# Performance work log

Hardware: AMD Instinct MI355X
Metric: run time of the kernel (lower is better)

The kernel has to match this reference:

```python
import jax, jax.numpy as jnp
import numpy as np


def setup_inputs() -> dict:
    key = jax.random.key(0)
    k1, k2 = jax.random.split(key)
    x = jax.random.normal(k1, (16, 512, 64, 64), dtype=jnp.float32)
    gamma = jax.random.normal(k2, (1,), dtype=jnp.float32) * 0.05  # 'random_normal' init
    return {"x": x, "gamma": gamma}


def reference(x, gamma):
    # x: (B, C, H, W); code path is channels_last, C taken from x.shape[1]
    B, C, H, W = x.shape
    N = H * W
    # Reshape((-1, C)) is a flat row-major reshape -> (B, N, C)
    q = x.reshape(B, N, C)  # query == key == value (same tensor)
    # energy = matmul(query, key, transpose_a=True) -> (B, C, C)
    energy = jnp.einsum('bnc,bnd->bcd', q, q)
    # reduce_max(energy, axis=1, keepdims=True)[0]: max over axis 1 then take
    # FIRST BATCH element -> shape (1, C), broadcast against (B, C, C)
    mx = jnp.max(energy, axis=1, keepdims=True)[0]  # (1, C)
    energy_2 = mx - energy  # (B, C, C)
    # Keras Activation('softmax') -> softmax over last axis
    attention = jax.nn.softmax(energy_2, axis=-1)  # (B, C, C)
    # matmul(attention, value, transpose_b=True): (B,C,C) @ (B,C,N) -> (B,C,N)
    out = jnp.einsum('bcd,bnd->bcn', attention, q)
    # Reshape back to x.shape[1:] = (C, H, W) (flat reshape, N = H*W)
    out = out.reshape(B, C, H, W)
    return gamma * out + x
```

## Files before the change

kernel.cpp:

```cpp
#include <hip/hip_runtime.h>
#include <cstdint>

#define B_DIM 16
#define C_DIM 512
#define N_DIM 4096

typedef __bf16 bf16x8 __attribute__((ext_vector_type(8)));
typedef unsigned short u16x8 __attribute__((ext_vector_type(8)));
typedef unsigned short u16x4 __attribute__((ext_vector_type(4)));
typedef float f32x4 __attribute__((ext_vector_type(4)));

__device__ __forceinline__ unsigned short f2bf_tr(float f) {
    return (unsigned short)(__float_as_uint(f) >> 16);
}
__device__ __forceinline__ bf16x8 as_bf(u16x8 v) {
    return __builtin_bit_cast(bf16x8, v);
}

#define BT 128
#define BK 32
#define BKP 40

__global__ __launch_bounds__(256) void gram_kernel(const float* __restrict__ x,
                                                   float* __restrict__ part, int kshift) {
    const int sk = 1 << kshift;
    const int s = blockIdx.z & (sk - 1);
    const int b = blockIdx.z >> kshift;
    static const int TI[10] = {0, 0, 0, 0, 1, 1, 1, 2, 2, 3};
    static const int TJ[10] = {0, 1, 2, 3, 1, 2, 3, 2, 3, 3};
    const int c0 = TI[blockIdx.x] * BT;
    const int d0 = TJ[blockIdx.x] * BT;
    const bool diag = (c0 == d0);

    const float* __restrict__ Q = x + (size_t)b * (N_DIM * C_DIM);
    float* __restrict__ E = part + ((size_t)s * B_DIM + b) * (C_DIM * C_DIM);

    __shared__ unsigned short lAh[BT][BKP];
    __shared__ unsigned short lAl[BT][BKP];
    __shared__ unsigned short lBh[BT][BKP];
    __shared__ unsigned short lBl[BT][BKP];

    const int tid = threadIdx.x;
    const int lane = tid & 63;
    const int w = tid >> 6;
    const int moff = (w & 1) * 64;
    const int noff = (w >> 1) * 64;
    const int frow = lane & 15;
    const int fk = (lane >> 4) * 8;

    f32x4 acc[4][4];
#pragma unroll
    for (int m = 0; m < 4; ++m)
#pragma unroll
        for (int n = 0; n < 4; ++n) acc[m][n] = (f32x4){0.f, 0.f, 0.f, 0.f};

    const int cc = tid & 127;
    const int kh = tid >> 7;

    const int klen = N_DIM >> kshift;
    const int kbeg = s * klen;
    const float* gA = Q + (size_t)(kbeg + kh * 16) * C_DIM + (c0 + cc);
    const float* gB = Q + (size_t)(kbeg + kh * 16) * C_DIM + (d0 + cc);

    const unsigned short(*pBh)[BKP] = diag ? lAh : lBh;
    const unsigned short(*pBl)[BKP] = diag ? lAl : lBl;

    for (int k0 = 0; k0 < klen; k0 += BK) {
        u16x8 vah[2], val[2], vbh[2], vbl[2];
#pragma unroll
        for (int i = 0; i < 16; ++i) {
            float fa = gA[(size_t)i * C_DIM];
            unsigned int ua = __float_as_uint(fa);
            unsigned short ah = (unsigned short)(ua >> 16);
            float rsa = fa - __uint_as_float(ua & 0xffff0000u);
            unsigned short al = (unsigned short)(__float_as_uint(rsa) >> 16);
            vah[i >> 3][i & 7] = ah;
            val[i >> 3][i & 7] = al;
        }
        if (!diag) {
#pragma unroll
            for (int i = 0; i < 16; ++i) {
                float fb = gB[(size_t)i * C_DIM];
                unsigned int ub = __float_as_uint(fb);
                unsigned short bh = (unsigned short)(ub >> 16);
                float rsb = fb - __uint_as_float(ub & 0xffff0000u);
                unsigned short bl = (unsigned short)(__float_as_uint(rsb) >> 16);
                vbh[i >> 3][i & 7] = bh;
                vbl[i >> 3][i & 7] = bl;
            }
        }
        gA += (size_t)BK * C_DIM;
        gB += (size_t)BK * C_DIM;

        __syncthreads();
        *(u16x8*)&lAh[cc][kh * 16]     = vah[0];
        *(u16x8*)&lAh[cc][kh * 16 + 8] = vah[1];
        *(u16x8*)&lAl[cc][kh * 16]     = val[0];
        *(u16x8*)&lAl[cc][kh * 16 + 8] = val[1];
        if (!diag) {
            *(u16x8*)&lBh[cc][kh * 16]     = vbh[0];
            *(u16x8*)&lBh[cc][kh * 16 + 8] = vbh[1];
            *(u16x8*)&lBl[cc][kh * 16]     = vbl[0];
            *(u16x8*)&lBl[cc][kh * 16 + 8] = vbl[1];
        }
        __syncthreads();

        bf16x8 fa_h[4], fa_l[4], fb_h[4], fb_l[4];
#pragma unroll
        for (int m = 0; m < 4; ++m) {
            fa_h[m] = as_bf(*(const u16x8*)&lAh[moff + m * 16 + frow][fk]);
            fa_l[m] = as_bf(*(const u16x8*)&lAl[moff + m * 16 + frow][fk]);
        }
#pragma unroll
        for (int n = 0; n < 4; ++n) {
            fb_h[n] = as_bf(*(const u16x8*)&pBh[noff + n * 16 + frow][fk]);
            fb_l[n] = as_bf(*(const u16x8*)&pBl[noff + n * 16 + frow][fk]);
        }
#pragma unroll
        for (int m = 0; m < 4; ++m)
#pragma unroll
            for (int n = 0; n < 4; ++n) {
                acc[m][n] = __builtin_amdgcn_mfma_f32_16x16x32_bf16(fa_h[m], fb_h[n], acc[m][n], 0, 0, 0);
                acc[m][n] = __builtin_amdgcn_mfma_f32_16x16x32_bf16(fa_h[m], fb_l[n], acc[m][n], 0, 0, 0);
                acc[m][n] = __builtin_amdgcn_mfma_f32_16x16x32_bf16(fa_l[m], fb_h[n], acc[m][n], 0, 0, 0);
            }
    }

#pragma unroll
    for (int m = 0; m < 4; ++m)
#pragma unroll
        for (int n = 0; n < 4; ++n) {
            const int r = c0 + moff + m * 16 + (lane >> 4) * 4;
            const int col = d0 + noff + n * 16 + frow;
#pragma unroll
            for (int i = 0; i < 4; ++i)
                E[(size_t)(r + i) * C_DIM + col] = acc[m][n][i];
        }
    if (!diag) {
#pragma unroll
        for (int m = 0; m < 4; ++m)
#pragma unroll
            for (int n = 0; n < 4; ++n) {
                const int r = c0 + moff + m * 16 + (lane >> 4) * 4;
                const int col = d0 + noff + n * 16 + frow;
#pragma unroll
                for (int i = 0; i < 4; ++i)
                    E[(size_t)col * C_DIM + (r + i)] = acc[m][n][i];
            }
    }
}

__global__ __launch_bounds__(256) void colmax1(const float* __restrict__ part,
                                               float* __restrict__ pmax, int sk) {
    const int d = blockIdx.x * 256 + threadIdx.x;
    const int cg = blockIdx.y;
    const size_t PS = (size_t)B_DIM * C_DIM * C_DIM;
    float m = -3.4e38f;
    for (int c = cg * 64; c < cg * 64 + 64; ++c) {
        float e = 0.f;
        for (int s = 0; s < sk; ++s) e += part[(size_t)s * PS + (size_t)c * C_DIM + d];
        m = fmaxf(m, e);
    }
    pmax[cg * C_DIM + d] = m;
}

__global__ __launch_bounds__(256) void colmax2(const float* __restrict__ pmax,
                                               float* __restrict__ mx) {
    const int d = blockIdx.x * 256 + threadIdx.x;
    float m = pmax[d];
#pragma unroll
    for (int g = 1; g < 8; ++g) m = fmaxf(m, pmax[g * C_DIM + d]);
    mx[d] = m;
}

__global__ __launch_bounds__(256) void softmax_kernel(float* __restrict__ part,
                                                      const float* __restrict__ mx, int sk) {
    const int wid = blockIdx.x * 4 + (threadIdx.x >> 6);
    const int lane = threadIdx.x & 63;
    const size_t PS = (size_t)B_DIM * C_DIM * C_DIM;

    f32x4 ea = (f32x4){0.f, 0.f, 0.f, 0.f}, eb = ea;
    for (int s = 0; s < sk; ++s) {
        const f32x4* row = (const f32x4*)(part + (size_t)s * PS + (size_t)wid * C_DIM + lane * 8);
        ea += row[0];
        eb += row[1];
    }
    f32x4 ma = *(const f32x4*)&mx[lane * 8];
    f32x4 mb = *(const f32x4*)&mx[lane * 8 + 4];

    float v[8];
#pragma unroll
    for (int j = 0; j < 4; ++j) v[j] = ma[j] - ea[j];
#pragma unroll
    for (int j = 0; j < 4; ++j) v[4 + j] = mb[j] - eb[j];

    float rm = v[0];
#pragma unroll
    for (int j = 1; j < 8; ++j) rm = fmaxf(rm, v[j]);
#pragma unroll
    for (int st = 1; st < 64; st <<= 1) rm = fmaxf(rm, __shfl_xor(rm, st));

    float p[8];
    float sum = 0.f;
#pragma unroll
    for (int j = 0; j < 8; ++j) {
        p[j] = expf(v[j] - rm);
        sum += p[j];
    }
#pragma unroll
    for (int st = 1; st < 64; st <<= 1) sum += __shfl_xor(sum, st);

    const float inv = 1.f / sum;
    f32x4 o0 = {p[0] * inv, p[1] * inv, p[2] * inv, p[3] * inv};
    f32x4 o1 = {p[4] * inv, p[5] * inv, p[6] * inv, p[7] * inv};
    f32x4* row0 = (f32x4*)(part + (size_t)wid * C_DIM + lane * 8);
    row0[0] = o0;
    row0[1] = o1;
}

__global__ __launch_bounds__(256) void gemm2_kernel(const float* __restrict__ att,
                                                    const float* __restrict__ x,
                                                    const float* __restrict__ gamma,
                                                    float* __restrict__ out) {
    const int b = blockIdx.z;
    const int c0 = blockIdx.x * BT;
    const int n0 = blockIdx.y * BT;
    const float* __restrict__ A = att + (size_t)b * (C_DIM * C_DIM);
    const float* __restrict__ Q = x + (size_t)b * (N_DIM * C_DIM);
    const float* __restrict__ Xb = Q;
    float* __restrict__ Ob = out + (size_t)b * (C_DIM * N_DIM);

    __shared__ unsigned short lA[BT][BKP];
    __shared__ unsigned short lB[BT][BKP];

    const int tid = threadIdx.x;
    const int lane = tid & 63;
    const int w = tid >> 6;
    const int moff = (w & 1) * 64;
    const int noff = (w >> 1) * 64;
    const int frow = lane & 15;
    const int fk = (lane >> 4) * 8;

    f32x4 acc[4][4];
#pragma unroll
    for (int m = 0; m < 4; ++m)
#pragma unroll
        for (int n = 0; n < 4; ++n) acc[m][n] = (f32x4){0.f, 0.f, 0.f, 0.f};

    for (int k0 = 0; k0 < C_DIM; k0 += BK) {
        float4 ra[4], rb[4];
#pragma unroll
        for (int i = 0; i < 4; ++i) {
            const int f = tid + 256 * i;
            const int rr = f >> 3;
            const int k4 = (f & 7) * 4;
            ra[i] = *(const float4*)&A[(size_t)(c0 + rr) * C_DIM + k0 + k4];
            rb[i] = *(const float4*)&Q[(size_t)(n0 + rr) * C_DIM + k0 + k4];
        }
        __syncthreads();
#pragma unroll
        for (int i = 0; i < 4; ++i) {
            const int f = tid + 256 * i;
            const int rr = f >> 3;
            const int k4 = (f & 7) * 4;
            u16x4 pa = {f2bf_tr(ra[i].x), f2bf_tr(ra[i].y), f2bf_tr(ra[i].z), f2bf_tr(ra[i].w)};
            u16x4 pb = {f2bf_tr(rb[i].x), f2bf_tr(rb[i].y), f2bf_tr(rb[i].z), f2bf_tr(rb[i].w)};
            *(u16x4*)&lA[rr][k4] = pa;
            *(u16x4*)&lB[rr][k4] = pb;
        }
        __syncthreads();

        bf16x8 fa[4], fb[4];
#pragma unroll
        for (int m = 0; m < 4; ++m)
            fa[m] = as_bf(*(const u16x8*)&lA[moff + m * 16 + frow][fk]);
#pragma unroll
        for (int n = 0; n < 4; ++n)
            fb[n] = as_bf(*(const u16x8*)&lB[noff + n * 16 + frow][fk]);
#pragma unroll
        for (int m = 0; m < 4; ++m)
#pragma unroll
            for (int n = 0; n < 4; ++n)
                acc[m][n] = __builtin_amdgcn_mfma_f32_16x16x32_bf16(fa[m], fb[n], acc[m][n], 0, 0, 0);
    }

    const float g = gamma[0];
#pragma unroll
    for (int m = 0; m < 4; ++m)
#pragma unroll
        for (int n = 0; n < 4; ++n) {
            const int r = c0 + moff + m * 16 + (lane >> 4) * 4;
            const int col = n0 + noff + n * 16 + frow;
#pragma unroll
            for (int i = 0; i < 4; ++i) {
                const size_t idx = (size_t)(r + i) * N_DIM + col;
                Ob[idx] = g * acc[m][n][i] + Xb[idx];
            }
        }
}

extern "C" void kernel_launch(void* const* d_in, const int* in_sizes, int n_in,
                              void* d_out, int out_size, void* d_ws, size_t ws_size,
                              hipStream_t stream) {
    const float* x = (const float*)d_in[0];
    const float* gamma = (const float*)d_in[1];
    float* out = (float*)d_out;

    const size_t HDR = 32 * 1024;
    const size_t PSZ = (size_t)B_DIM * C_DIM * C_DIM * sizeof(float);
    int kshift = 0;
    if (ws_size >= HDR + 4 * PSZ) kshift = 2;
    else if (ws_size >= HDR + 2 * PSZ) kshift = 1;
    const int SK = 1 << kshift;

    float* mx = (float*)d_ws;
    float* pmax = mx + C_DIM;
    float* part = (float*)((char*)d_ws + HDR);

    dim3 g1(10, 1, B_DIM * SK);
    gram_kernel<<<g1, 256, 0, stream>>>(x, part, kshift);

    colmax1<<<dim3(2, 8), 256, 0, stream>>>(part, pmax, SK);
    colmax2<<<2, 256, 0, stream>>>(pmax, mx);

    softmax_kernel<<<(B_DIM * C_DIM) / 4, 256, 0, stream>>>(part, mx, SK);

    dim3 g2(C_DIM / BT, N_DIM / BT, B_DIM);
    gemm2_kernel<<<g2, 256, 0, stream>>>(part, x, gamma, out);
}
```

Before: 291.0 us.

## Prefetch gram/GEMM tiles, store attention as bf16, swizzle workgroup order

The gram kernel now loads the next K-slab into registers while MFMAs run on the current slab, packs hi/lo bf16 with byte-perm, and remaps workgroups with an XCD-aware swizzle. Softmax writes the attention as round-to-nearest bf16 in place, into the upper half of each fp32 row. gemm2 reads that bf16 directly and double-buffers shared memory with register prefetch, using the same swizzled block order. The aim is to hide global-load latency, halve attention traffic and improve L2 locality, at the cost of more registers and an in-place aliasing trick in the workspace.

New measurement: 634.6 us. +118.0%, slower.

```diff
diff --git a/kernel.cpp b/kernel.cpp
--- a/kernel.cpp
+++ b/kernel.cpp
@@ -8,28 +8,41 @@
 typedef __bf16 bf16x8 __attribute__((ext_vector_type(8)));
 typedef unsigned short u16x8 __attribute__((ext_vector_type(8)));
 typedef unsigned short u16x4 __attribute__((ext_vector_type(4)));
+typedef unsigned int u32x4 __attribute__((ext_vector_type(4)));
+typedef unsigned int u32x2 __attribute__((ext_vector_type(2)));
 typedef float f32x4 __attribute__((ext_vector_type(4)));
 
-__device__ __forceinline__ unsigned short f2bf_tr(float f) {
-    return (unsigned short)(__float_as_uint(f) >> 16);
-}
-__device__ __forceinline__ bf16x8 as_bf(u16x8 v) {
-    return __builtin_bit_cast(bf16x8, v);
+__device__ __forceinline__ bf16x8 as_bf(u16x8 v) { return __builtin_bit_cast(bf16x8, v); }
+
+__device__ __forceinline__ unsigned pack_hi(unsigned ua, unsigned ub) {
+    return __builtin_amdgcn_perm(ub, ua, 0x07060302u);
+}
+__device__ __forceinline__ unsigned rne_pack(float a, float b) {
+    unsigned ua = __float_as_uint(a);
+    ua += 0x7fffu + ((ua >> 16) & 1u);
+    unsigned ub = __float_as_uint(b);
+    ub += 0x7fffu + ((ub >> 16) & 1u);
+    return pack_hi(ua, ub);
 }
 
 #define BT 128
 #define BK 32
 #define BKP 40
 
-__global__ __launch_bounds__(256) void gram_kernel(const float* __restrict__ x,
-                                                   float* __restrict__ part, int kshift) {
-    const int sk = 1 << kshift;
-    const int s = blockIdx.z & (sk - 1);
-    const int b = blockIdx.z >> kshift;
+__global__ __launch_bounds__(256, 4) void gram_kernel(const float* __restrict__ x,
+                                                      float* __restrict__ part, int kshift) {
+    const int nwg = 10 * gridDim.z;
+    const int chunk = nwg >> 3;
+    const int flat = blockIdx.x + 10 * blockIdx.z;
+    const int swz = (flat & 7) * chunk + (flat >> 3);
+    const int tile = swz % 10;
+    const int z = swz / 10;
+    const int s = z & ((1 << kshift) - 1);
+    const int b = z >> kshift;
     static const int TI[10] = {0, 0, 0, 0, 1, 1, 1, 2, 2, 3};
     static const int TJ[10] = {0, 1, 2, 3, 1, 2, 3, 2, 3, 3};
-    const int c0 = TI[blockIdx.x] * BT;
-    const int d0 = TJ[blockIdx.x] * BT;
+    const int c0 = TI[tile] * BT;
+    const int d0 = TJ[tile] * BT;
     const bool diag = (c0 == d0);
 
     const float* __restrict__ Q = x + (size_t)b * (N_DIM * C_DIM);
@@ -58,72 +71,91 @@
     const int kh = tid >> 7;
 
     const int klen = N_DIM >> kshift;
-    const int kbeg = s * klen;
-    const float* gA = Q + (size_t)(kbeg + kh * 16) * C_DIM + (c0 + cc);
-    const float* gB = Q + (size_t)(kbeg + kh * 16) * C_DIM + (d0 + cc);
+    const float* gA = Q + (size_t)(s * klen + kh * 16) * C_DIM + (c0 + cc);
+    const float* gB = Q + (size_t)(s * klen + kh * 16) * C_DIM + (d0 + cc);
 
     const unsigned short(*pBh)[BKP] = diag ? lAh : lBh;
     const unsigned short(*pBl)[BKP] = diag ? lAl : lBl;
 
-    for (int k0 = 0; k0 < klen; k0 += BK) {
-        u16x8 vah[2], val[2], vbh[2], vbl[2];
-#pragma unroll
-        for (int i = 0; i < 16; ++i) {
-            float fa = gA[(size_t)i * C_DIM];
-            unsigned int ua = __float_as_uint(fa);
-            unsigned short ah = (unsigned short)(ua >> 16);
-            float rsa = fa - __uint_as_float(ua & 0xffff0000u);
-            unsigned short al = (unsigned short)(__float_as_uint(rsa) >> 16);
-            vah[i >> 3][i & 7] = ah;
-            val[i >> 3][i & 7] = al;
-        }
+    float av[16], bv[16];
+#pragma unroll
+    for (int i = 0; i < 16; ++i) av[i] = gA[(size_t)i * C_DIM];
+    if (!diag) {
+#pragma unroll
+        for (int i = 0; i < 16; ++i) bv[i] = gB[(size_t)i * C_DIM];
+    }
+    gA += (size_t)BK * C_DIM;
+    gB += (size_t)BK * C_DIM;
+
+    const int T = klen / BK;
+    for (int t = 0; t < T; ++t) {
+        u32x4 ah[2], al[2], bh[2], bl[2];
+#pragma unroll
+        for (int g = 0; g < 2; ++g)
+#pragma unroll
+            for (int p = 0; p < 4; ++p) {
+                const int j = g * 8 + p * 2;
+                unsigned u0 = __float_as_uint(av[j]), u1 = __float_as_uint(av[j + 1]);
+                ah[g][p] = pack_hi(u0, u1);
+                float r0 = av[j] - __uint_as_float(u0 & 0xffff0000u);
+                float r1 = av[j + 1] - __uint_as_float(u1 & 0xffff0000u);
+                al[g][p] = pack_hi(__float_as_uint(r0), __float_as_uint(r1));
+            }
         if (!diag) {
 #pragma unroll
-            for (int i = 0; i < 16; ++i) {
-                float fb = gB[(size_t)i * C_DIM];
-                unsigned int ub = __float_as_uint(fb);
-                unsigned short bh = (unsigned short)(ub >> 16);
-                float rsb = fb - __uint_as_float(ub & 0xffff0000u);
-                unsigned short bl = (unsigned short)(__float_as_uint(rsb) >> 16);
-                vbh[i >> 3][i & 7] = bh;
-                vbl[i >> 3][i & 7] = bl;
-            }
-        }
-        gA += (size_t)BK * C_DIM;
-        gB += (size_t)BK * C_DIM;
+            for (int g = 0; g < 2; ++g)
+#pragma unroll
+                for (int p = 0; p < 4; ++p) {
+                    const int j = g * 8 + p * 2;
+                    unsigned u0 = __float_as_uint(bv[j]), u1 = __float_as_uint(bv[j + 1]);
+                    bh[g][p] = pack_hi(u0, u1);
+                    float r0 = bv[j] - __uint_as_float(u0 & 0xffff0000u);
+                    float r1 = bv[j + 1] - __uint_as_float(u1 & 0xffff0000u);
+                    bl[g][p] = pack_hi(__float_as_uint(r0), __float_as_uint(r1));
+                }
+        }
 
         __syncthreads();
-        *(u16x8*)&lAh[cc][kh * 16]     = vah[0];
-        *(u16x8*)&lAh[cc][kh * 16 + 8] = vah[1];
-        *(u16x8*)&lAl[cc][kh * 16]     = val[0];
-        *(u16x8*)&lAl[cc][kh * 16 + 8] = val[1];
+        *(u16x8*)&lAh[cc][kh * 16]     = __builtin_bit_cast(u16x8, ah[0]);
+        *(u16x8*)&lAh[cc][kh * 16 + 8] = __builtin_bit_cast(u16x8, ah[1]);
+        *(u16x8*)&lAl[cc][kh * 16]     = __builtin_bit_cast(u16x8, al[0]);
+        *(u16x8*)&lAl[cc][kh * 16 + 8] = __builtin_bit_cast(u16x8, al[1]);
         if (!diag) {
-            *(u16x8*)&lBh[cc][kh * 16]     = vbh[0];
-            *(u16x8*)&lBh[cc][kh * 16 + 8] = vbh[1];
-            *(u16x8*)&lBl[cc][kh * 16]     = vbl[0];
-            *(u16x8*)&lBl[cc][kh * 16 + 8] = vbl[1];
+            *(u16x8*)&lBh[cc][kh * 16]     = __builtin_bit_cast(u16x8, bh[0]);
+            *(u16x8*)&lBh[cc][kh * 16 + 8] = __builtin_bit_cast(u16x8, bh[1]);
+            *(u16x8*)&lBl[cc][kh * 16]     = __builtin_bit_cast(u16x8, bl[0]);
+            *(u16x8*)&lBl[cc][kh * 16 + 8] = __builtin_bit_cast(u16x8, bl[1]);
         }
         __syncthreads();
 
-        bf16x8 fa_h[4], fa_l[4], fb_h[4], fb_l[4];
+        if (t + 1 < T) {
+#pragma unroll
+            for (int i = 0; i < 16; ++i) av[i] = gA[(size_t)i * C_DIM];
+            if (!diag) {
+#pragma unroll
+                for (int i = 0; i < 16; ++i) bv[i] = gB[(size_t)i * C_DIM];
+            }
+            gA += (size_t)BK * C_DIM;
+            gB += (size_t)BK * C_DIM;
+        }
+
+        bf16x8 fbh[4], fbl[4];
+#pragma unroll
+        for (int n = 0; n < 4; ++n) {
+            fbh[n] = as_bf(*(const u16x8*)&pBh[noff + n * 16 + frow][fk]);
+            fbl[n] = as_bf(*(const u16x8*)&pBl[noff + n * 16 + frow][fk]);
+        }
 #pragma unroll
         for (int m = 0; m < 4; ++m) {
-            fa_h[m] = as_bf(*(const u16x8*)&lAh[moff + m * 16 + frow][fk]);
-            fa_l[m] = as_bf(*(const u16x8*)&lAl[moff + m * 16 + frow][fk]);
-        }
-#pragma unroll
-        for (int n = 0; n < 4; ++n) {
-            fb_h[n] = as_bf(*(const u16x8*)&pBh[noff + n * 16 + frow][fk]);
-            fb_l[n] = as_bf(*(const u16x8*)&pBl[noff + n * 16 + frow][fk]);
-        }
-#pragma unroll
-        for (int m = 0; m < 4; ++m)
+            bf16x8 fah = as_bf(*(const u16x8*)&lAh[moff + m * 16 + frow][fk]);
+            bf16x8 fal = as_bf(*(const u16x8*)&lAl[moff + m * 16 + frow][fk]);
 #pragma unroll
             for (int n = 0; n < 4; ++n) {
-                acc[m][n] = __builtin_amdgcn_mfma_f32_16x16x32_bf16(fa_h[m], fb_h[n], acc[m][n], 0, 0, 0);
-                acc[m][n] = __builtin_amdgcn_mfma_f32_16x16x32_bf16(fa_h[m], fb_l[n], acc[m][n], 0, 0, 0);
-                acc[m][n] = __builtin_amdgcn_mfma_f32_16x16x32_bf16(fa_l[m], fb_h[n], acc[m][n], 0, 0, 0);
-            }
+                acc[m][n] = __builtin_amdgcn_mfma_f32_16x16x32_bf16(fah, fbh[n], acc[m][n], 0, 0, 0);
+                acc[m][n] = __builtin_amdgcn_mfma_f32_16x16x32_bf16(fah, fbl[n], acc[m][n], 0, 0, 0);
+                acc[m][n] = __builtin_amdgcn_mfma_f32_16x16x32_bf16(fal, fbh[n], acc[m][n], 0, 0, 0);
+            }
+        }
     }
 
 #pragma unroll
@@ -211,27 +243,30 @@
     for (int st = 1; st < 64; st <<= 1) sum += __shfl_xor(sum, st);
 
     const float inv = 1.f / sum;
-    f32x4 o0 = {p[0] * inv, p[1] * inv, p[2] * inv, p[3] * inv};
-    f32x4 o1 = {p[4] * inv, p[5] * inv, p[6] * inv, p[7] * inv};
-    f32x4* row0 = (f32x4*)(part + (size_t)wid * C_DIM + lane * 8);
-    row0[0] = o0;
-    row0[1] = o1;
-}
-
-__global__ __launch_bounds__(256) void gemm2_kernel(const float* __restrict__ att,
-                                                    const float* __restrict__ x,
-                                                    const float* __restrict__ gamma,
-                                                    float* __restrict__ out) {
-    const int b = blockIdx.z;
-    const int c0 = blockIdx.x * BT;
-    const int n0 = blockIdx.y * BT;
-    const float* __restrict__ A = att + (size_t)b * (C_DIM * C_DIM);
+    u32x4 o;
+#pragma unroll
+    for (int q = 0; q < 4; ++q) o[q] = rne_pack(p[2 * q] * inv, p[2 * q + 1] * inv);
+    unsigned short* arow = (unsigned short*)part + (size_t)wid * 1024 + 512;
+    *(u16x8*)&arow[lane * 8] = __builtin_bit_cast(u16x8, o);
+}
+
+__global__ __launch_bounds__(256, 4) void gemm2_kernel(const unsigned short* __restrict__ att16,
+                                                       const float* __restrict__ x,
+                                                       const float* __restrict__ gamma,
+                                                       float* __restrict__ out) {
+    const int flat = blockIdx.x + 4 * (blockIdx.y + 32 * blockIdx.z);
+    const int swz = (flat & 7) * 256 + (flat >> 3);
+    const int c0 = (swz & 3) * BT;
+    const int n0 = ((swz >> 2) & 31) * BT;
+    const int b = swz >> 7;
+
     const float* __restrict__ Q = x + (size_t)b * (N_DIM * C_DIM);
     const float* __restrict__ Xb = Q;
     float* __restrict__ Ob = out + (size_t)b * (C_DIM * N_DIM);
-
-    __shared__ unsigned short lA[BT][BKP];
-    __shared__ unsigned short lB[BT][BKP];
+    const unsigned short* __restrict__ Ab = att16 + (size_t)(b * C_DIM + c0) * 1024 + 512;
+
+    __shared__ unsigned short lA[2][BT][BKP];
+    __shared__ unsigned short lB[2][BT][BKP];
 
     const int tid = threadIdx.x;
     const int lane = tid & 63;
@@ -247,41 +282,76 @@
 #pragma unroll
         for (int n = 0; n < 4; ++n) acc[m][n] = (f32x4){0.f, 0.f, 0.f, 0.f};
 
-    for (int k0 = 0; k0 < C_DIM; k0 += BK) {
-        float4 ra[4], rb[4];
-#pragma unroll
-        for (int i = 0; i < 4; ++i) {
-            const int f = tid + 256 * i;
-            const int rr = f >> 3;
-            const int k4 = (f & 7) * 4;
-            ra[i] = *(const float4*)&A[(size_t)(c0 + rr) * C_DIM + k0 + k4];
-            rb[i] = *(const float4*)&Q[(size_t)(n0 + rr) * C_DIM + k0 + k4];
-        }
+    u16x8 pa[2];
+    float4 rb[4];
+#pragma unroll
+    for (int i = 0; i < 2; ++i) {
+        const int f = tid + 256 * i;
+        pa[i] = *(const u16x8*)&Ab[(size_t)(f >> 2) * 1024 + ((f & 3) * 8)];
+    }
+#pragma unroll
+    for (int i = 0; i < 4; ++i) {
+        const int f = tid + 256 * i;
+        rb[i] = *(const float4*)&Q[(size_t)(n0 + (f >> 3)) * C_DIM + ((f & 7) * 4)];
+    }
+#pragma unroll
+    for (int i = 0; i < 2; ++i) {
+        const int f = tid + 256 * i;
+        *(u16x8*)&lA[0][f >> 2][(f & 3) * 8] = pa[i];
+    }
+#pragma unroll
+    for (int i = 0; i < 4; ++i) {
+        const int f = tid + 256 * i;
+        u32x2 pk = {pack_hi(__float_as_uint(rb[i].x), __float_as_uint(rb[i].y)),
+                    pack_hi(__float_as_uint(rb[i].z), __float_as_uint(rb[i].w))};
+        *(u16x4*)&lB[0][f >> 3][(f & 7) * 4] = __builtin_bit_cast(u16x4, pk);
+    }
+
+    int cur = 0;
+    for (int t = 0; t < 16; ++t) {
         __syncthreads();
-#pragma unroll
-        for (int i = 0; i < 4; ++i) {
-            const int f = tid + 256 * i;
-            const int rr = f >> 3;
-            const int k4 = (f & 7) * 4;
-            u16x4 pa = {f2bf_tr(ra[i].x), f2bf_tr(ra[i].y), f2bf_tr(ra[i].z), f2bf_tr(ra[i].w)};
-            u16x4 pb = {f2bf_tr(rb[i].x), f2bf_tr(rb[i].y), f2bf_tr(rb[i].z), f2bf_tr(rb[i].w)};
-            *(u16x4*)&lA[rr][k4] = pa;
-            *(u16x4*)&lB[rr][k4] = pb;
-        }
-        __syncthreads();
-
-        bf16x8 fa[4], fb[4];
-#pragma unroll
-        for (int m = 0; m < 4; ++m)
-            fa[m] = as_bf(*(const u16x8*)&lA[moff + m * 16 + frow][fk]);
+        if (t < 15) {
+            const int k1 = (t + 1) * BK;
+#pragma unroll
+            for (int i = 0; i < 2; ++i) {
+                const int f = tid + 256 * i;
+                pa[i] = *(const u16x8*)&Ab[(size_t)(f >> 2) * 1024 + k1 + ((f & 3) * 8)];
+            }
+#pragma unroll
+            for (int i = 0; i < 4; ++i) {
+                const int f = tid + 256 * i;
+                rb[i] = *(const float4*)&Q[(size_t)(n0 + (f >> 3)) * C_DIM + k1 + ((f & 7) * 4)];
+            }
+        }
+
+        bf16x8 fb[4];
 #pragma unroll
         for (int n = 0; n < 4; ++n)
-            fb[n] = as_bf(*(const u16x8*)&lB[noff + n * 16 + frow][fk]);
-#pragma unroll
-        for (int m = 0; m < 4; ++m)
+            fb[n] = as_bf(*(const u16x8*)&lB[cur][noff + n * 16 + frow][fk]);
+#pragma unroll
+        for (int m = 0; m < 4; ++m) {
+            bf16x8 fa = as_bf(*(const u16x8*)&lA[cur][moff + m * 16 + frow][fk]);
 #pragma unroll
             for (int n = 0; n < 4; ++n)
-                acc[m][n] = __builtin_amdgcn_mfma_f32_16x16x32_bf16(fa[m], fb[n], acc[m][n], 0, 0, 0);
+                acc[m][n] = __builtin_amdgcn_mfma_f32_16x16x32_bf16(fa, fb[n], acc[m][n], 0, 0, 0);
+        }
+
+        if (t < 15) {
+            const int nb = cur ^ 1;
+#pragma unroll
+            for (int i = 0; i < 2; ++i) {
+                const int f = tid + 256 * i;
+                *(u16x8*)&lA[nb][f >> 2][(f & 3) * 8] = pa[i];
+            }
+#pragma unroll
+            for (int i = 0; i < 4; ++i) {
+                const int f = tid + 256 * i;
+                u32x2 pk = {pack_hi(__float_as_uint(rb[i].x), __float_as_uint(rb[i].y)),
+                            pack_hi(__float_as_uint(rb[i].z), __float_as_uint(rb[i].w))};
+                *(u16x4*)&lB[nb][f >> 3][(f & 7) * 4] = __builtin_bit_cast(u16x4, pk);
+            }
+        }
+        cur ^= 1;
     }
 
     const float g = gamma[0];
@@ -326,5 +396,5 @@
     softmax_kernel<<<(B_DIM * C_DIM) / 4, 256, 0, stream>>>(part, mx, SK);
 
     dim3 g2(C_DIM / BT, N_DIM / BT, B_DIM);
-    gemm2_kernel<<<g2, 256, 0, stream>>>(part, x, gamma, out);
-}
+    gemm2_kernel<<<g2, 256, 0, stream>>>((const unsigned short*)part, x, gamma, out);
+}
```
